# Performance work log

Measured on AMD Instinct MI355X. Metric: run time of the kernel, lower is better.

Reference implementation:

```python
import jax, jax.numpy as jnp
import numpy as np

N_NODES = 100000
N_EDGES = 3200000
IN_CH = 256
HID = 256   # 2 * out_channels
OUT = 128


def _gcn_norm(edge_index, n):
    # PyG GCNConv normalization: add self-loops, norm = d^-1/2[src] * d^-1/2[dst]
    src, dst = edge_index[0], edge_index[1]
    loops = jnp.arange(n, dtype=src.dtype)
    src = jnp.concatenate([src, loops])
    dst = jnp.concatenate([dst, loops])
    ones = jnp.ones_like(dst, dtype=jnp.float32)
    deg = jax.ops.segment_sum(ones, dst, num_segments=n)
    dinv = jnp.where(deg > 0, jax.lax.rsqrt(deg), 0.0)
    norm = dinv[src] * dinv[dst]
    return src, dst, norm


def _gcn_conv(x, W, b, src, dst, norm, n):
    h = x @ W                              # [N, F_out] dense transform first (F_out <= F_in)
    msg = h[src] * norm[:, None]           # gather + scale  [E+N, F_out]
    out = jax.ops.segment_sum(msg, dst, num_segments=n)  # scatter-add
    return out + b


def setup_inputs() -> dict:
    key = jax.random.key(0)
    k1, k2, k3, k4 = jax.random.split(key, 4)
    x = jax.random.normal(k1, (N_NODES, IN_CH), dtype=jnp.float32)
    edge_index = jax.random.randint(k2, (2, N_EDGES), 0, N_NODES, dtype=jnp.int64)
    # Glorot-style init for weights, zero bias (PyG GCNConv defaults)
    W1 = jax.random.normal(k3, (IN_CH, HID), dtype=jnp.float32) * (1.0 / np.sqrt(IN_CH))
    b1 = jnp.zeros((HID,), dtype=jnp.float32)
    W2 = jax.random.normal(k4, (HID, OUT), dtype=jnp.float32) * (1.0 / np.sqrt(HID))
    b2 = jnp.zeros((OUT,), dtype=jnp.float32)
    return {"x": x, "edge_index": edge_index, "W1": W1, "b1": b1, "W2": W2, "b2": b2}


def reference(x, edge_index, W1, b1, W2, b2):
    n = x.shape[0]
    src, dst, norm = _gcn_norm(edge_index, n)  # cached=True: shared across both layers
    h = _gcn_conv(x, W1, b1, src, dst, norm, n)
    h = jax.nn.relu(h)
    z = _gcn_conv(h, W2, b2, src, dst, norm, n)
    return z
```

## Files before the change

kernel.cpp:

```cpp
#include <hip/hip_runtime.h>
#include <cstdio>


#define NPB 256
#define PCHUNK 8192

template <int V> struct vec_t;
template <> struct vec_t<2> {
  typedef float    fv __attribute__((ext_vector_type(2)));
  typedef _Float16 hv __attribute__((ext_vector_type(2)));
};
template <> struct vec_t<4> {
  typedef float    fv __attribute__((ext_vector_type(4)));
  typedef _Float16 hv __attribute__((ext_vector_type(4)));
};
typedef _Float16 half4v __attribute__((ext_vector_type(4)));
typedef _Float16 half8v __attribute__((ext_vector_type(8)));
typedef float    f32x4  __attribute__((ext_vector_type(4)));

__global__ __launch_bounds__(256) void k_zero(int* p, int n) {
  int i = blockIdx.x * 256 + threadIdx.x;
  if (i < n) p[i] = 0;
}

__global__ __launch_bounds__(256) void k_bhist(const int* __restrict__ dst,
                                               int* __restrict__ bcnt,
                                               int e, int nb) {
  __shared__ int h[512];
  for (int i = threadIdx.x; i < nb; i += 256) h[i] = 0;
  __syncthreads();
  int c0 = blockIdx.x * PCHUNK;
  int c1 = min(c0 + PCHUNK, e);
  for (int i = c0 + threadIdx.x; i < c1; i += 256)
    atomicAdd(&h[dst[i] >> 8], 1);
  __syncthreads();
  for (int i = threadIdx.x; i < nb; i += 256)
    if (h[i]) atomicAdd(&bcnt[i], h[i]);
}

__global__ __launch_bounds__(512) void k_bscan(const int* __restrict__ bcnt,
                                               int* __restrict__ bbase,
                                               int* __restrict__ gcur, int nb) {
  __shared__ int sm[512];
  int tid = threadIdx.x;
  sm[tid] = (tid < nb) ? bcnt[tid] : 0;
  __syncthreads();
  for (int d = 1; d < 512; d <<= 1) {
    int t = (tid >= d) ? sm[tid - d] : 0;
    __syncthreads();
    sm[tid] += t;
    __syncthreads();
  }
  int ex = (tid == 0) ? 0 : sm[tid - 1];
  if (tid < nb) {
    bbase[tid] = ex;
    gcur[tid] = ex;
  }
  if (tid == nb) bbase[nb] = sm[nb - 1];
}

__global__ __launch_bounds__(256) void k_partition(const int* __restrict__ src,
                                                   const int* __restrict__ dst,
                                                   int* __restrict__ gcur,
                                                   uint2* __restrict__ tmp,
                                                   int e, int nb) {
  __shared__ int hist[512];
  __shared__ int base[512];
  for (int i = threadIdx.x; i < nb; i += 256) hist[i] = 0;
  __syncthreads();
  int c0 = blockIdx.x * PCHUNK;
  int c1 = min(c0 + PCHUNK, e);
  for (int i = c0 + threadIdx.x; i < c1; i += 256)
    atomicAdd(&hist[dst[i] >> 8], 1);
  __syncthreads();
  for (int i = threadIdx.x; i < nb; i += 256) {
    int c = hist[i];
    base[i] = c ? atomicAdd(&gcur[i], c) : 0;
    hist[i] = 0;
  }
  __syncthreads();
  for (int i = c0 + threadIdx.x; i < c1; i += 256) {
    int d = dst[i];
    int b = d >> 8;
    int pos = base[b] + atomicAdd(&hist[b], 1);
    uint2 v;
    v.x = (unsigned)src[i];
    v.y = (unsigned)d;
    tmp[pos] = v;
  }
}

__global__ __launch_bounds__(256) void k_bucket(const uint2* __restrict__ tmp,
                                                const int* __restrict__ bbase,
                                                int* __restrict__ off,
                                                float* __restrict__ dinv,
                                                int* __restrict__ esrc, int n) {
  __shared__ int lcnt[NPB];
  __shared__ int lsum[NPB];
  __shared__ int lcur[NPB];
  const int b = blockIdx.x;
  const int tid = threadIdx.x;
  const int r0 = b << 8;
  const int nn = min(NPB, n - r0);
  const int lo = bbase[b], hi = bbase[b + 1];

  lcnt[tid] = 0;
  __syncthreads();
  for (int i = lo + tid; i < hi; i += 256)
    atomicAdd(&lcnt[tmp[i].y & (NPB - 1)], 1);
  __syncthreads();
  lsum[tid] = lcnt[tid];
  __syncthreads();
  for (int d = 1; d < NPB; d <<= 1) {
    int t = (tid >= d) ? lsum[tid - d] : 0;
    __syncthreads();
    lsum[tid] += t;
    __syncthreads();
  }
  int ex = (tid == 0) ? 0 : lsum[tid - 1];
  if (tid < nn) {
    off[r0 + tid] = lo + ex;
    dinv[r0 + tid] = rsqrtf((float)(lcnt[tid] + 1));
    lcur[tid] = lo + ex;
  }
  if (r0 + nn == n && tid == 0) off[n] = hi;
  __syncthreads();
  for (int i = lo + tid; i < hi; i += 256) {
    uint2 t2 = tmp[i];
    int pos = atomicAdd(&lcur[t2.y & (NPB - 1)], 1);
    esrc[pos] = (int)t2.x;
  }
}

__global__ __launch_bounds__(256) void k_castWT(const float* __restrict__ W,
                                                _Float16* __restrict__ WhT,
                                                _Float16* __restrict__ WlT,
                                                int K, int N) {
  int i = blockIdx.x * 256 + threadIdx.x;
  if (i >= K * N) return;
  int n = i % N, k = i / N;
  float v = W[i];
  _Float16 h = (_Float16)v;
  WhT[(size_t)n * K + k] = h;
  WlT[(size_t)n * K + k] = (_Float16)(v - (float)h);
}

template <typename AT, int NTERMS>
__global__ __launch_bounds__(256, 2) void k_gemm_mfma(
    const AT* __restrict__ A, const _Float16* __restrict__ BhT,
    const _Float16* __restrict__ BlT, _Float16* __restrict__ C,
    int M, int N, int K) {
  constexpr bool SPLITA = (NTERMS == 3);
  __shared__ _Float16 Ah[128][40];
  __shared__ _Float16 Al[SPLITA ? 128 : 1][40];

  const int tid = threadIdx.x;
  const int bm = blockIdx.x * 128;
  const int bn = blockIdx.y * 128;

  const int arow = tid >> 1;
  const int acol = (tid & 1) * 16;
  const bool avalid = (bm + arow) < M;
  const AT* aptr = A + (size_t)(bm + arow) * K + acol;

  const int wave = tid >> 6, lane = tid & 63;
  const int wm = (wave & 1) * 64, wn = (wave >> 1) * 64;
  const int lr = lane & 15, quad = lane >> 4;

  const _Float16* bh0 = BhT + (size_t)(bn + wn + lr) * K + quad * 8;
  const _Float16* bl0 = BlT + (size_t)(bn + wn + lr) * K + quad * 8;

  f32x4 acc[4][4] = {};

  for (int k0 = 0; k0 < K; k0 += 32) {
    __syncthreads();
    if (avalid) {
#pragma unroll
      for (int ii = 0; ii < 4; ++ii) {
        if constexpr (SPLITA) {
          f32x4 v = *(const f32x4*)(aptr + k0 + ii * 4);
          half4v hv, lv;
#pragma unroll
          for (int j = 0; j < 4; ++j) {
            hv[j] = (_Float16)v[j];
            lv[j] = (_Float16)(v[j] - (float)hv[j]);
          }
          *(half4v*)&Ah[arow][acol + ii * 4] = hv;
          *(half4v*)&Al[arow][acol + ii * 4] = lv;
        } else {
          half4v v = *(const half4v*)(aptr + k0 + ii * 4);
          *(half4v*)&Ah[arow][acol + ii * 4] = v;
        }
      }
    } else {
      half4v z = {};
#pragma unroll
      for (int ii = 0; ii < 4; ++ii) {
        *(half4v*)&Ah[arow][acol + ii * 4] = z;
        if constexpr (SPLITA) *(half4v*)&Al[arow][acol + ii * 4] = z;
      }
    }
    __syncthreads();

    half8v af[4], alf[4], bhf[4], blf[4];
#pragma unroll
    for (int mi = 0; mi < 4; ++mi) {
      af[mi] = *(const half8v*)&Ah[wm + mi * 16 + lr][quad * 8];
      if constexpr (SPLITA)
        alf[mi] = *(const half8v*)&Al[wm + mi * 16 + lr][quad * 8];
    }
#pragma unroll
    for (int ni = 0; ni < 4; ++ni) {
      bhf[ni] = *(const half8v*)(bh0 + (size_t)(ni * 16) * K + k0);
      blf[ni] = *(const half8v*)(bl0 + (size_t)(ni * 16) * K + k0);
    }
#pragma unroll
    for (int mi = 0; mi < 4; ++mi)
#pragma unroll
      for (int ni = 0; ni < 4; ++ni) {
        acc[mi][ni] = __builtin_amdgcn_mfma_f32_16x16x32_f16(
            af[mi], bhf[ni], acc[mi][ni], 0, 0, 0);
        acc[mi][ni] = __builtin_amdgcn_mfma_f32_16x16x32_f16(
            af[mi], blf[ni], acc[mi][ni], 0, 0, 0);
        if constexpr (SPLITA)
          acc[mi][ni] = __builtin_amdgcn_mfma_f32_16x16x32_f16(
              alf[mi], bhf[ni], acc[mi][ni], 0, 0, 0);
      }
  }

#pragma unroll
  for (int mi = 0; mi < 4; ++mi)
#pragma unroll
    for (int r = 0; r < 4; ++r) {
      int row = bm + wm + mi * 16 + quad * 4 + r;
      if (row < M) {
#pragma unroll
        for (int ni = 0; ni < 4; ++ni)
          C[(size_t)row * N + bn + wn + ni * 16 + lr] =
              (_Float16)acc[mi][ni][r];
      }
    }
}

template <int C, bool RELU, typename OutT>
__global__ __launch_bounds__(256) void k_agg(const _Float16* __restrict__ h,
                                             const int* __restrict__ esrc,
                                             const int* __restrict__ off,
                                             const float* __restrict__ dinv,
                                             const float* __restrict__ bias,
                                             OutT* __restrict__ out, int n) {
  constexpr int V = C / 64;
  typedef typename vec_t<V>::fv FV;
  typedef typename vec_t<V>::hv HV;
  int gwave = (blockIdx.x * 256 + threadIdx.x) >> 6;
  int lane = threadIdx.x & 63;
  if (gwave >= n) return;
  const int i = gwave;
  const float di = dinv[i];

  FV acc = di * __builtin_convertvector(
                    *(const HV*)(h + (size_t)i * C + lane * V), FV);

  int e = off[i];
  const int e1 = off[i + 1];
  for (; e + 3 < e1; e += 4) {
    int s0 = esrc[e], s1 = esrc[e + 1], s2 = esrc[e + 2], s3 = esrc[e + 3];
    float w0 = dinv[s0], w1 = dinv[s1], w2 = dinv[s2], w3 = dinv[s3];
    HV v0 = *(const HV*)(h + (size_t)s0 * C + lane * V);
    HV v1 = *(const HV*)(h + (size_t)s1 * C + lane * V);
    HV v2 = *(const HV*)(h + (size_t)s2 * C + lane * V);
    HV v3 = *(const HV*)(h + (size_t)s3 * C + lane * V);
    acc += w0 * __builtin_convertvector(v0, FV);
    acc += w1 * __builtin_convertvector(v1, FV);
    acc += w2 * __builtin_convertvector(v2, FV);
    acc += w3 * __builtin_convertvector(v3, FV);
  }
  for (; e < e1; ++e) {
    int s = esrc[e];
    acc += dinv[s] * __builtin_convertvector(
                         *(const HV*)(h + (size_t)s * C + lane * V), FV);
  }

  FV bv = *(const FV*)(bias + lane * V);
  FV r = acc * di + bv;
  if (RELU) {
#pragma unroll
    for (int v = 0; v < V; ++v) r[v] = fmaxf(r[v], 0.f);
  }
  if constexpr (sizeof(OutT) == 2) {
    *(HV*)(out + (size_t)i * C + lane * V) = __builtin_convertvector(r, HV);
  } else {
    *(FV*)(out + (size_t)i * C + lane * V) = r;
  }
}

extern "C" void kernel_launch(void* const* d_in, const int* in_sizes, int n_in,
                              void* d_out, int out_size, void* d_ws, size_t ws_size,
                              hipStream_t stream) {
  const float* x  = (const float*)d_in[0];
  const int*   ei = (const int*)d_in[1];
  const float* W1 = (const float*)d_in[2];
  const float* b1 = (const float*)d_in[3];
  const float* W2 = (const float*)d_in[4];
  const float* b2 = (const float*)d_in[5];
  float* out = (float*)d_out;

  const int IN_CH = 256, HID = 256, OUT = 128;
  const int N = in_sizes[0] / IN_CH;
  const int E = in_sizes[1] / 2;
  const int* src = ei;
  const int* dst = ei + E;
  const int NB = (N + NPB - 1) / NPB;

  char* p = (char*)d_ws;
  auto alloc = [&](size_t bytes) {
    void* r = (void*)p;
    p += (bytes + 255) & ~(size_t)255;
    return r;
  };
  _Float16* h1   = (_Float16*)alloc((size_t)N * HID * 2);
  _Float16* h1r  = (_Float16*)alloc((size_t)N * HID * 2);
  int*      esrc = (int*)alloc((size_t)E * 4);
  uint2*    tmp  = (uint2*)alloc((size_t)E * 8);
  int*      off  = (int*)alloc((size_t)(N + 1) * 4);
  float*    dinv = (float*)alloc((size_t)N * 4);
  int*      bcnt = (int*)alloc((size_t)(NB + 1) * 4);
  int*      bbase= (int*)alloc((size_t)(NB + 1) * 4);
  int*      gcur = (int*)alloc((size_t)(NB + 1) * 4);
  _Float16* w1h  = (_Float16*)alloc((size_t)IN_CH * HID * 2);
  _Float16* w1l  = (_Float16*)alloc((size_t)IN_CH * HID * 2);
  _Float16* w2h  = (_Float16*)alloc((size_t)HID * OUT * 2);
  _Float16* w2l  = (_Float16*)alloc((size_t)HID * OUT * 2);
  if ((size_t)(p - (char*)d_ws) > ws_size) {
    fprintf(stderr, "kernel_launch: ws too small (need %zu, have %zu)\n",
            (size_t)(p - (char*)d_ws), ws_size);
    return;
  }

  const int nBlkP = (E + PCHUNK - 1) / PCHUNK;

  k_zero<<<(NB + 255) / 256, 256, 0, stream>>>(bcnt, NB);
  k_bhist<<<nBlkP, 256, 0, stream>>>(dst, bcnt, E, NB);
  k_bscan<<<1, 512, 0, stream>>>(bcnt, bbase, gcur, NB);
  k_partition<<<nBlkP, 256, 0, stream>>>(src, dst, gcur, tmp, E, NB);
  k_bucket<<<NB, 256, 0, stream>>>(tmp, bbase, off, dinv, esrc, N);
  k_castWT<<<(IN_CH * HID + 255) / 256, 256, 0, stream>>>(W1, w1h, w1l, IN_CH, HID);
  k_castWT<<<(HID * OUT + 255) / 256, 256, 0, stream>>>(W2, w2h, w2l, HID, OUT);
  dim3 g1((N + 127) / 128, HID / 128);
  k_gemm_mfma<float, 3><<<g1, 256, 0, stream>>>(x, w1h, w1l, h1, N, HID, IN_CH);
  int aggBlk = (N + 3) / 4;
  k_agg<256, true, _Float16><<<aggBlk, 256, 0, stream>>>(h1, esrc, off, dinv, b1, h1r, N);
  dim3 g2((N + 127) / 128, OUT / 128);
  k_gemm_mfma<_Float16, 2><<<g2, 256, 0, stream>>>(h1r, w2h, w2l, h1, N, OUT, HID);
  k_agg<128, false, float><<<aggBlk, 256, 0, stream>>>(h1, esrc, off, dinv, b2, out, N);
}
```

Baseline: 746.9 us.

## Aggregate before transform in layer one and fuse bias-ReLU into GEMM

Layer one now casts x to fp16, aggregates neighbours on the raw features, then multiplies by W1 with bias and ReLU fused into the GEMM epilogue. This uses associativity of the normalized adjacency and the weight. The GEMM drops its split-A low-precision term, cutting MFMA work by a third, and the two weight-cast launches are merged into one. The trade-offs are an extra full pass that casts x to half, and lower precision from rounding x to fp16 before aggregation.

```diff
diff --git a/kernel.cpp b/kernel.cpp
--- a/kernel.cpp
+++ b/kernel.cpp
@@ -132,27 +132,45 @@
   }
 }
 
-__global__ __launch_bounds__(256) void k_castWT(const float* __restrict__ W,
-                                                _Float16* __restrict__ WhT,
-                                                _Float16* __restrict__ WlT,
-                                                int K, int N) {
+__global__ __launch_bounds__(256) void k_castX(const float* __restrict__ x,
+                                               _Float16* __restrict__ xh,
+                                               int n4) {
   int i = blockIdx.x * 256 + threadIdx.x;
-  if (i >= K * N) return;
-  int n = i % N, k = i / N;
-  float v = W[i];
-  _Float16 h = (_Float16)v;
-  WhT[(size_t)n * K + k] = h;
-  WlT[(size_t)n * K + k] = (_Float16)(v - (float)h);
-}
-
-template <typename AT, int NTERMS>
+  if (i >= n4) return;
+  f32x4 v = *(const f32x4*)(x + (size_t)i * 4);
+  half4v h;
+#pragma unroll
+  for (int j = 0; j < 4; ++j) h[j] = (_Float16)v[j];
+  *(half4v*)(xh + (size_t)i * 4) = h;
+}
+
+__global__ __launch_bounds__(256) void k_castW(
+    const float* __restrict__ W1, const float* __restrict__ W2,
+    _Float16* __restrict__ w1h, _Float16* __restrict__ w1l,
+    _Float16* __restrict__ w2h, _Float16* __restrict__ w2l) {
+  int i = blockIdx.x * 256 + threadIdx.x;
+  if (i < 256 * 256) {
+    int n = i & 255, k = i >> 8;
+    float v = W1[i];
+    _Float16 h = (_Float16)v;
+    w1h[(size_t)n * 256 + k] = h;
+    w1l[(size_t)n * 256 + k] = (_Float16)(v - (float)h);
+  } else if (i < 256 * 256 + 256 * 128) {
+    int j = i - 256 * 256;
+    int n = j & 127, k = j >> 7;
+    float v = W2[j];
+    _Float16 h = (_Float16)v;
+    w2h[(size_t)n * 256 + k] = h;
+    w2l[(size_t)n * 256 + k] = (_Float16)(v - (float)h);
+  }
+}
+
+template <bool BIASRELU>
 __global__ __launch_bounds__(256, 2) void k_gemm_mfma(
-    const AT* __restrict__ A, const _Float16* __restrict__ BhT,
-    const _Float16* __restrict__ BlT, _Float16* __restrict__ C,
-    int M, int N, int K) {
-  constexpr bool SPLITA = (NTERMS == 3);
+    const _Float16* __restrict__ A, const _Float16* __restrict__ BhT,
+    const _Float16* __restrict__ BlT, const float* __restrict__ bias,
+    _Float16* __restrict__ C, int M, int N, int K) {
   __shared__ _Float16 Ah[128][40];
-  __shared__ _Float16 Al[SPLITA ? 128 : 1][40];
 
   const int tid = threadIdx.x;
   const int bm = blockIdx.x * 128;
@@ -161,7 +179,7 @@
   const int arow = tid >> 1;
   const int acol = (tid & 1) * 16;
   const bool avalid = (bm + arow) < M;
-  const AT* aptr = A + (size_t)(bm + arow) * K + acol;
+  const _Float16* aptr = A + (size_t)(bm + arow) * K + acol;
 
   const int wave = tid >> 6, lane = tid & 63;
   const int wm = (wave & 1) * 64, wn = (wave >> 1) * 64;
@@ -176,39 +194,21 @@
     __syncthreads();
     if (avalid) {
 #pragma unroll
-      for (int ii = 0; ii < 4; ++ii) {
-        if constexpr (SPLITA) {
-          f32x4 v = *(const f32x4*)(aptr + k0 + ii * 4);
-          half4v hv, lv;
-#pragma unroll
-          for (int j = 0; j < 4; ++j) {
-            hv[j] = (_Float16)v[j];
-            lv[j] = (_Float16)(v[j] - (float)hv[j]);
-          }
-          *(half4v*)&Ah[arow][acol + ii * 4] = hv;
-          *(half4v*)&Al[arow][acol + ii * 4] = lv;
-        } else {
-          half4v v = *(const half4v*)(aptr + k0 + ii * 4);
-          *(half4v*)&Ah[arow][acol + ii * 4] = v;
-        }
-      }
+      for (int ii = 0; ii < 4; ++ii)
+        *(half4v*)&Ah[arow][acol + ii * 4] =
+            *(const half4v*)(aptr + k0 + ii * 4);
     } else {
       half4v z = {};
 #pragma unroll
-      for (int ii = 0; ii < 4; ++ii) {
+      for (int ii = 0; ii < 4; ++ii)
         *(half4v*)&Ah[arow][acol + ii * 4] = z;
-        if constexpr (SPLITA) *(half4v*)&Al[arow][acol + ii * 4] = z;
-      }
     }
     __syncthreads();
 
-    half8v af[4], alf[4], bhf[4], blf[4];
-#pragma unroll
-    for (int mi = 0; mi < 4; ++mi) {
+    half8v af[4], bhf[4], blf[4];
+#pragma unroll
+    for (int mi = 0; mi < 4; ++mi)
       af[mi] = *(const half8v*)&Ah[wm + mi * 16 + lr][quad * 8];
-      if constexpr (SPLITA)
-        alf[mi] = *(const half8v*)&Al[wm + mi * 16 + lr][quad * 8];
-    }
 #pragma unroll
     for (int ni = 0; ni < 4; ++ni) {
       bhf[ni] = *(const half8v*)(bh0 + (size_t)(ni * 16) * K + k0);
@@ -222,12 +222,15 @@
             af[mi], bhf[ni], acc[mi][ni], 0, 0, 0);
         acc[mi][ni] = __builtin_amdgcn_mfma_f32_16x16x32_f16(
             af[mi], blf[ni], acc[mi][ni], 0, 0, 0);
-        if constexpr (SPLITA)
-          acc[mi][ni] = __builtin_amdgcn_mfma_f32_16x16x32_f16(
-              alf[mi], bhf[ni], acc[mi][ni], 0, 0, 0);
       }
   }
 
+  float bv[4] = {0.f, 0.f, 0.f, 0.f};
+  if (BIASRELU) {
+#pragma unroll
+    for (int ni = 0; ni < 4; ++ni)
+      bv[ni] = bias[bn + wn + ni * 16 + lr];
+  }
 #pragma unroll
   for (int mi = 0; mi < 4; ++mi)
 #pragma unroll
@@ -235,14 +238,16 @@
       int row = bm + wm + mi * 16 + quad * 4 + r;
       if (row < M) {
 #pragma unroll
-        for (int ni = 0; ni < 4; ++ni)
-          C[(size_t)row * N + bn + wn + ni * 16 + lr] =
-              (_Float16)acc[mi][ni][r];
+        for (int ni = 0; ni < 4; ++ni) {
+          float v = acc[mi][ni][r];
+          if (BIASRELU) v = fmaxf(v + bv[ni], 0.f);
+          C[(size_t)row * N + bn + wn + ni * 16 + lr] = (_Float16)v;
+        }
       }
     }
 }
 
-template <int C, bool RELU, typename OutT>
+template <int C, bool RELU, bool HASBIAS, typename OutT>
 __global__ __launch_bounds__(256) void k_agg(const _Float16* __restrict__ h,
                                              const int* __restrict__ esrc,
                                              const int* __restrict__ off,
@@ -281,8 +286,8 @@
                          *(const HV*)(h + (size_t)s * C + lane * V), FV);
   }
 
-  FV bv = *(const FV*)(bias + lane * V);
-  FV r = acc * di + bv;
+  FV r = acc * di;
+  if (HASBIAS) r += *(const FV*)(bias + lane * V);
   if (RELU) {
 #pragma unroll
     for (int v = 0; v < V; ++v) r[v] = fmaxf(r[v], 0.f);
@@ -318,8 +323,8 @@
     p += (bytes + 255) & ~(size_t)255;
     return r;
   };
-  _Float16* h1   = (_Float16*)alloc((size_t)N * HID * 2);
-  _Float16* h1r  = (_Float16*)alloc((size_t)N * HID * 2);
+  _Float16* xh   = (_Float16*)alloc((size_t)N * IN_CH * 2);
+  _Float16* xa   = (_Float16*)alloc((size_t)N * IN_CH * 2);
   int*      esrc = (int*)alloc((size_t)E * 4);
   uint2*    tmp  = (uint2*)alloc((size_t)E * 8);
   int*      off  = (int*)alloc((size_t)(N + 1) * 4);
@@ -336,6 +341,8 @@
             (size_t)(p - (char*)d_ws), ws_size);
     return;
   }
+  _Float16* h1r = xh;
+  _Float16* h2  = xa;
 
   const int nBlkP = (E + PCHUNK - 1) / PCHUNK;
 
@@ -344,13 +351,17 @@
   k_bscan<<<1, 512, 0, stream>>>(bcnt, bbase, gcur, NB);
   k_partition<<<nBlkP, 256, 0, stream>>>(src, dst, gcur, tmp, E, NB);
   k_bucket<<<NB, 256, 0, stream>>>(tmp, bbase, off, dinv, esrc, N);
-  k_castWT<<<(IN_CH * HID + 255) / 256, 256, 0, stream>>>(W1, w1h, w1l, IN_CH, HID);
-  k_castWT<<<(HID * OUT + 255) / 256, 256, 0, stream>>>(W2, w2h, w2l, HID, OUT);
+  int n4 = N * IN_CH / 4;
+  k_castX<<<(n4 + 255) / 256, 256, 0, stream>>>(x, xh, n4);
+  k_castW<<<(256 * 256 + 256 * 128 + 255) / 256, 256, 0, stream>>>(
+      W1, W2, w1h, w1l, w2h, w2l);
+  int aggBlk = (N + 3) / 4;
+  k_agg<256, false, false, _Float16><<<aggBlk, 256, 0, stream>>>(
+      xh, esrc, off, dinv, nullptr, xa, N);
   dim3 g1((N + 127) / 128, HID / 128);
-  k_gemm_mfma<float, 3><<<g1, 256, 0, stream>>>(x, w1h, w1l, h1, N, HID, IN_CH);
-  int aggBlk = (N + 3) / 4;
-  k_agg<256, true, _Float16><<<aggBlk, 256, 0, stream>>>(h1, esrc, off, dinv, b1, h1r, N);
+  k_gemm_mfma<true><<<g1, 256, 0, stream>>>(xa, w1h, w1l, b1, h1r, N, HID, IN_CH);
   dim3 g2((N + 127) / 128, OUT / 128);
-  k_gemm_mfma<_Float16, 2><<<g2, 256, 0, stream>>>(h1r, w2h, w2l, h1, N, OUT, HID);
-  k_agg<128, false, float><<<aggBlk, 256, 0, stream>>>(h1, esrc, off, dinv, b2, out, N);
-}
+  k_gemm_mfma<false><<<g2, 256, 0, stream>>>(h1r, w2h, w2l, nullptr, h2, N, OUT, HID);
+  k_agg<128, false, true, float><<<aggBlk, 256, 0, stream>>>(
+      h2, esrc, off, dinv, b2, out, N);
+}
```

Result: slower. 766.0 us (+2.6%).
